# Optimization experiments

Hardware: AMD Instinct MI355X
Metric: run time of the kernel (lower is better)

The kernel has to match this reference:

```python
import jax, jax.numpy as jnp
import numpy as np

MC = 64  # mc_samples; fill=1.0 -> k == k_ball so neighbor ordering is irrelevant


def swish(x):
    return x * jax.nn.sigmoid(x)


def setup_inputs() -> dict:
    key = jax.random.key(0)
    ks = jax.random.split(key, 12)
    bs, n, g_dim = 4, 1024, 6
    c_in = c_out = 256
    H, hid = 8, 16

    def lin(k, i, o):
        return (jax.random.normal(k, (i, o), jnp.float32) / np.sqrt(i).astype(np.float32))

    return {
        "pairwise_g": jax.random.normal(ks[0], (bs, n, n, g_dim), jnp.float32),
        "coset_functions": jax.random.normal(ks[1], (bs, n, c_in), jnp.float32),
        "mask": jax.random.randint(ks[2], (bs, n), 0, 2) > 0,
        # per-head location-kernel MLP (MultiheadWeightNet: g_dim -> hid -> hid -> 1)
        "loc_W1": jax.random.normal(ks[3], (H, g_dim, hid), jnp.float32) / np.sqrt(g_dim).astype(np.float32),
        "loc_b1": jnp.zeros((H, hid), jnp.float32),
        "loc_W2": jax.random.normal(ks[4], (H, hid, hid), jnp.float32) / np.sqrt(hid).astype(np.float32),
        "loc_b2": jnp.zeros((H, hid), jnp.float32),
        "loc_W3": jax.random.normal(ks[5], (H, hid, 1), jnp.float32) / np.sqrt(hid).astype(np.float32),
        "loc_b3": jnp.zeros((H, 1), jnp.float32),
        # DotProductKernel projections
        "Wq": lin(ks[6], c_in, c_in), "bq": jnp.zeros((c_in,), jnp.float32),
        "Wk": lin(ks[7], c_in, c_in), "bk": jnp.zeros((c_in,), jnp.float32),
        # value (input_linear) and output projections
        "W_in": lin(ks[8], c_in, c_out), "b_in": jnp.zeros((c_out,), jnp.float32),
        "W_out": lin(ks[9], c_out, c_out), "b_out": jnp.zeros((c_out,), jnp.float32),
    }


def reference(pairwise_g, coset_functions, mask, loc_W1, loc_b1, loc_W2, loc_b2,
              loc_W3, loc_b3, Wq, bq, Wk, bk, W_in, b_in, W_out, b_out):
    bs, n, _, g_dim = pairwise_g.shape
    c_in = coset_functions.shape[-1]
    H = loc_W1.shape[0]
    dh = c_in // H
    b_idx = jnp.arange(bs)[:, None, None]

    # --- neighbourhood extraction: topk (smallest) group distances, masked keys pushed far away
    dists = jnp.linalg.norm(pairwise_g, axis=-1)                  # (b,n,n)
    dists = jnp.where(mask[:, None, :], dists, jnp.float32(1e8))
    _, nbhd_idx = jax.lax.top_k(-dists, MC)                       # (b,n,m) nearest MC keys
    nbhd_g = jnp.take_along_axis(pairwise_g, nbhd_idx[..., None], axis=2)  # (b,n,m,g)
    nbhd_mask = mask[b_idx, nbhd_idx]                             # (b,n,m)

    # --- location kernel: per-head MLP on gathered pairwise group elements
    h = swish(jnp.einsum('bnmg,hgk->bnmhk', nbhd_g, loc_W1) + loc_b1)
    h = swish(jnp.einsum('bnmhk,hkl->bnmhl', h, loc_W2) + loc_b2)
    loc = swish(jnp.einsum('bnmhk,hko->bnmho', h, loc_W3) + loc_b3)[..., 0]  # (b,n,m,H)

    # --- feature kernel: dot-product scores on gathered keys
    q = (coset_functions @ Wq + bq).reshape(bs, n, H, dh)
    k = (coset_functions @ Wk + bk).reshape(bs, n, H, dh)
    k_nbhd = k[b_idx, nbhd_idx]                                   # (b,n,m,H,dh)
    feat = jnp.einsum('bnhd,bnmhd->bnmh', q, k_nbhd) / np.sqrt(dh).astype(np.float32)

    # --- masked softmax over the neighbourhood dim (dim 2)
    scores = jnp.where(nbhd_mask[..., None], loc + feat, jnp.float32(-1e38))
    attn = jax.nn.softmax(scores, axis=2)                         # (b,n,m,H)

    # --- value projection + sparse attention (equivalent to the dense scatter+matmul,
    #     since topk neighbour indices are unique per query)
    v = (coset_functions @ W_in + b_in).reshape(bs, n, H, dh)
    v_nbhd = v[b_idx, nbhd_idx]                                   # (b,n,m,H,dh)
    out = jnp.einsum('bnmh,bnmhd->bnhd', attn, v_nbhd).reshape(bs, n, H * dh)
    out = out @ W_out + b_out
    return (pairwise_g, out, mask)
```

## Files before the change

### kernel.cpp

```cpp
#include <hip/hip_runtime.h>
#include <stdint.h>

#define BS 4
#define NN 1024
#define GD 6
#define CIN 256
#define NH 8
#define DH 32
#define HID 16
#define MCS 64

#define PG_ELEMS (BS*NN*NN*GD)
#define OUT_OFF  PG_ELEMS
#define MASK_OFF (PG_ELEMS + BS*NN*CIN)

typedef float vfloat4 __attribute__((ext_vector_type(4)));
typedef float vfloat2 __attribute__((ext_vector_type(2)));
typedef unsigned vuint4 __attribute__((ext_vector_type(4)));

#if __has_builtin(__builtin_amdgcn_rcpf)
__device__ __forceinline__ float fast_rcp(float x) { return __builtin_amdgcn_rcpf(x); }
#else
__device__ __forceinline__ float fast_rcp(float x) { return 1.0f / x; }
#endif
#if __has_builtin(__builtin_amdgcn_exp2f)
__device__ __forceinline__ float fast_exp2(float x) { return __builtin_amdgcn_exp2f(x); }
#else
__device__ __forceinline__ float fast_exp2(float x) { return exp2f(x); }
#endif
#define LOG2E 1.44269504088896340736f

__device__ __forceinline__ float swishf(float x) {
    return x * fast_rcp(1.0f + fast_exp2(x * -LOG2E));
}

template<int RPB>
__global__ __launch_bounds__(256) void gemm3(const float* __restrict__ X,
    const float* __restrict__ W0, const float* __restrict__ B0, float* __restrict__ D0,
    const float* __restrict__ W1, const float* __restrict__ B1, float* __restrict__ D1,
    const float* __restrict__ W2, const float* __restrict__ B2, float* __restrict__ D2)
{
    const float* W; const float* Bv; float* D;
    if (blockIdx.y == 0)      { W = W0; Bv = B0; D = D0; }
    else if (blockIdx.y == 1) { W = W1; Bv = B1; D = D1; }
    else                      { W = W2; Bv = B2; D = D2; }
    const int tid = threadIdx.x;
    const int c4  = tid & 63;
    const int rg  = tid >> 6;
    const int r0  = blockIdx.x * RPB;
    constexpr int RG = RPB / 4;

    __shared__ float xsT[CIN][RPB + 4];
    {
        float tmp[RPB];
        #pragma unroll
        for (int r = 0; r < RPB; ++r) tmp[r] = X[(size_t)(r0 + r)*CIN + tid];
        #pragma unroll
        for (int j = 0; j < RPB/4; ++j)
            *(vfloat4*)&xsT[tid][4*j] = (vfloat4){tmp[4*j+0], tmp[4*j+1], tmp[4*j+2], tmp[4*j+3]};
    }
    __syncthreads();

    vfloat4 acc[RG];
    #pragma unroll
    for (int r = 0; r < RG; ++r) acc[r] = (vfloat4){0.f,0.f,0.f,0.f};
    const vfloat4* W4 = (const vfloat4*)W;
    #pragma unroll 4
    for (int k = 0; k < CIN; ++k) {
        vfloat4 w = W4[(size_t)k*64 + c4];
        if constexpr (RG == 4) {
            vfloat4 xr = *(const vfloat4*)&xsT[k][rg*4];
            acc[0] += xr.x * w;
            acc[1] += xr.y * w;
            acc[2] += xr.z * w;
            acc[3] += xr.w * w;
        } else {
            vfloat2 xr = *(const vfloat2*)&xsT[k][rg*2];
            acc[0] += xr.x * w;
            acc[1] += xr.y * w;
        }
    }
    vfloat4 bb = ((const vfloat4*)Bv)[c4];
    vfloat4* D4 = (vfloat4*)D;
    const size_t rbase = (size_t)(r0 + rg*RG);
    #pragma unroll
    for (int r = 0; r < RG; ++r) D4[(rbase + r)*64 + c4] = acc[r] + bb;
}

__global__ __launch_bounds__(256, 8) void attn_topk(
    const float* __restrict__ pg, const int* __restrict__ mask,
    const float* __restrict__ lW1g, const float* __restrict__ lb1g,
    const float* __restrict__ lW2g, const float* __restrict__ lb2g,
    const float* __restrict__ lW3g, const float* __restrict__ lb3g,
    const float* __restrict__ Q, const float* __restrict__ Kc, const float* __restrict__ Vc,
    float* __restrict__ O, float* __restrict__ pg_out, float* __restrict__ mask_out)
{
    const int i = blockIdx.x, b = blockIdx.y, tid = threadIdx.x;
    const int lane = tid & 63;

    __shared__ __align__(16) unsigned selbuf[512];
    __shared__ float sg[MCS*7];
    __shared__ int nj[MCS];
    __shared__ __align__(16) unsigned joff[MCS];
    __shared__ vfloat4 obuf[4][64];
    __shared__ unsigned wsum[4];
    __shared__ unsigned sel_bin, sel_need, sel_cnt2, s_cnt, s_eqcnt, s_cand;

    float (*sc)[NH]   = (float (*)[NH])selbuf;
    unsigned* hist    = selbuf;
    unsigned* eqlist  = selbuf + 256;

    const int* mrow = mask + b*NN;
    if (tid == 0) { mask_out[b*NN + i] = mrow[i] ? 1.0f : 0.0f; s_cand = 0; }

    const size_t rowoff = (size_t)(b*NN + i) * (NN*GD);
    const vfloat4* src4 = (const vfloat4*)(pg + rowoff);
    vfloat4* dst4 = (vfloat4*)(pg_out + rowoff);
    #pragma unroll
    for (int t = 0; t < 6; ++t) {
        vfloat4 v = src4[tid + 256*t];
        __builtin_nontemporal_store(v, &dst4[tid + 256*t]);
    }
    vfloat4 q4 = ((const vfloat4*)Q)[(size_t)(b*NN + i)*64 + (tid & 63)];

    const int4 mv = ((const int4*)mrow)[tid];
    const vfloat4* gg = src4 + tid*6;
    vfloat4 g0 = gg[0], g1 = gg[1], g2 = gg[2], g3 = gg[3], g4 = gg[4], g5 = gg[5];
    float rv[4][6];
    rv[0][0]=g0.x; rv[0][1]=g0.y; rv[0][2]=g0.z; rv[0][3]=g0.w; rv[0][4]=g1.x; rv[0][5]=g1.y;
    rv[1][0]=g1.z; rv[1][1]=g1.w; rv[1][2]=g2.x; rv[1][3]=g2.y; rv[1][4]=g2.z; rv[1][5]=g2.w;
    rv[2][0]=g3.x; rv[2][1]=g3.y; rv[2][2]=g3.z; rv[2][3]=g3.w; rv[2][4]=g4.x; rv[2][5]=g4.y;
    rv[3][0]=g4.z; rv[3][1]=g4.w; rv[3][2]=g5.x; rv[3][3]=g5.y; rv[3][4]=g5.z; rv[3][5]=g5.w;
    const int vb[4] = { mv.x, mv.y, mv.z, mv.w };
    unsigned key[4];
    #pragma unroll
    for (int r = 0; r < 4; ++r) {
        float d2 = rv[r][0]*rv[r][0] + rv[r][1]*rv[r][1] + rv[r][2]*rv[r][2]
                 + rv[r][3]*rv[r][3] + rv[r][4]*rv[r][4] + rv[r][5]*rv[r][5];
        key[r] = __float_as_uint(vb[r] ? d2 : 1e30f);
    }

    unsigned prefix = 0;
    int need = MCS;
    unsigned T = 0;
    int needT = 0;
    for (int level = 0; level < 4; ++level) {
        const int shift = 24 - 8*level;
        hist[tid] = 0;
        __syncthreads();
        if (level == 0) {
            #pragma unroll
            for (int r = 0; r < 4; ++r) {
                unsigned d = key[r] >> 24;
                unsigned long long todo = __ballot(true);
                while (todo) {
                    int leader = (int)(__ffsll((unsigned long long)todo) - 1);
                    unsigned dl = __shfl(d, leader);
                    unsigned long long match = __ballot(d == dl);
                    if (lane == leader) atomicAdd(&hist[dl], (unsigned)__popcll(match));
                    todo &= ~match;
                }
            }
        } else {
            const unsigned pmask = 0xFFFFFFFFu << (shift + 8);
            #pragma unroll
            for (int r = 0; r < 4; ++r)
                if ((key[r] & pmask) == prefix)
                    atomicAdd(&hist[(key[r] >> shift) & 0xFFu], 1u);
        }
        __syncthreads();
        unsigned own = hist[tid];
        unsigned v = own;
        #pragma unroll
        for (int off = 1; off < 64; off <<= 1) {
            unsigned nv = __shfl_up(v, off);
            if (lane >= off) v += nv;
        }
        if (lane == 63) wsum[tid >> 6] = v;
        __syncthreads();
        unsigned basec = 0;
        for (int w = 0; w < (tid >> 6); ++w) basec += wsum[w];
        unsigned incl = v + basec;
        unsigned excl = incl - own;
        if (excl < (unsigned)need && (unsigned)need <= incl) {
            sel_bin  = (unsigned)tid;
            sel_need = (unsigned)need - excl;
            sel_cnt2 = own;
        }
        __syncthreads();
        prefix |= (sel_bin << shift);
        need = (int)sel_need;
        if (level == 3) { T = prefix; needT = need; break; }
        const int bincnt = (int)sel_cnt2;
        if (bincnt <= 64) {
            const unsigned pmask = 0xFFFFFFFFu << shift;
            unsigned* ckey = selbuf + 256;
            #pragma unroll
            for (int r = 0; r < 4; ++r) {
                if ((key[r] & pmask) == prefix) {
                    unsigned u = atomicAdd(&s_cand, 1u);
                    ckey[u] = key[r];
                }
            }
            __syncthreads();
            if (tid < 64) {
                unsigned myk = (tid < bincnt) ? ckey[tid] : 0xFFFFFFFFu;
                int rr = 0, ee = 0;
                for (int t = 0; t < bincnt; ++t) {
                    unsigned kt = __shfl(myk, t);
                    rr += (kt <  myk) ? 1 : 0;
                    ee += (kt == myk) ? 1 : 0;
                }
                if (tid < bincnt && rr < need && need <= rr + ee) {
                    sel_bin  = myk;
                    sel_need = (unsigned)(need - rr);
                }
            }
            __syncthreads();
            T = sel_bin; needT = (int)sel_need;
            break;
        }
    }

    if (tid == 0) { s_cnt = 0; s_eqcnt = 0; }
    __syncthreads();
    #pragma unroll
    for (int r = 0; r < 4; ++r) {
        unsigned kk = key[r];
        int j = tid*4 + r;
        if (kk < T) {
            unsigned p = atomicAdd(&s_cnt, 1u);
            nj[p] = j | (vb[r] ? 0 : (int)0x80000000);
            #pragma unroll
            for (int g = 0; g < GD; ++g) sg[p*7 + g] = rv[r][g];
        } else if (kk == T) {
            unsigned e = atomicAdd(&s_eqcnt, 1u);
            if (e < 64) eqlist[e] = (unsigned)j;
        }
    }
    __syncthreads();
    const int cbase = (int)s_cnt;
    if (tid == 0) {
        int ec = (int)s_eqcnt; if (ec > 64) ec = 64;
        for (int s2 = 0; s2 < needT; ++s2) {
            int bi = -1, bj = 0x7FFFFFFF;
            for (int e = 0; e < ec; ++e) {
                int jj = (int)eqlist[e];
                if (jj < bj) { bj = jj; bi = e; }
            }
            if (bi >= 0) {
                eqlist[bi] = 0x7FFFFFFFu;
                nj[cbase + s2] = bj | (mrow[bj] ? 0 : (int)0x80000000);
            }
        }
    }
    __syncthreads();
    #pragma unroll
    for (int r = 0; r < 4; ++r) {
        if (key[r] == T) {
            int j = tid*4 + r;
            for (int s2 = 0; s2 < needT; ++s2)
                if ((nj[cbase + s2] & 0x7FFFFFFF) == j) {
                    #pragma unroll
                    for (int g = 0; g < GD; ++g) sg[(cbase + s2)*7 + g] = rv[r][g];
                }
        }
    }
    if (tid < MCS) joff[tid] = ((unsigned)(b*NN + (nj[tid] & 0x7FFFFFFF))) << 6;
    __syncthreads();

    __builtin_amdgcn_s_setprio(1);
    #pragma unroll
    for (int pass = 0; pass < 2; ++pass) {
        const int h = __builtin_amdgcn_readfirstlane((tid >> 6) + pass*4);
        const int m = lane;
        const float* W1h = lW1g + h*(GD*HID);
        const float* B1h = lb1g + h*HID;
        const float* W2h = lW2g + h*(HID*HID);
        const float* B2h = lb2g + h*HID;
        const float* W3h = lW3g + h*HID;
        float gv[GD];
        #pragma unroll
        for (int g = 0; g < GD; ++g) gv[g] = sg[m*7 + g];
        float h1[HID];
        #pragma unroll
        for (int kk = 0; kk < HID; ++kk) {
            float a = B1h[kk];
            #pragma unroll
            for (int g = 0; g < GD; ++g) a += gv[g] * W1h[g*HID + kk];
            h1[kk] = swishf(a);
        }
        float h2[HID];
        #pragma unroll
        for (int l = 0; l < HID; ++l) {
            float a = B2h[l];
            #pragma unroll
            for (int kk = 0; kk < HID; ++kk) a += h1[kk] * W2h[kk*HID + l];
            h2[l] = swishf(a);
        }
        float a3 = lb3g[h];
        #pragma unroll
        for (int kk = 0; kk < HID; ++kk) a3 += h2[kk] * W3h[kk];
        sc[m][h] = (nj[m] < 0) ? -1e38f : swishf(a3);
    }
    __syncthreads();

    const int q = tid & 63;
    const int p = tid >> 6;
    const int hh = q >> 3;
    q4 *= 0.17677669529663688f;
    const vfloat4* Kc4 = (const vfloat4*)Kc;
    const vuint4* jo4 = (const vuint4*)(joff + (p << 4));
    #pragma unroll
    for (int mg = 0; mg < 4; ++mg) {
        vuint4 o4 = jo4[mg];
        vfloat4 kv0 = Kc4[o4.x + (unsigned)q];
        vfloat4 kv1 = Kc4[o4.y + (unsigned)q];
        vfloat4 kv2 = Kc4[o4.z + (unsigned)q];
        vfloat4 kv3 = Kc4[o4.w + (unsigned)q];
        const int mb = (p << 4) + (mg << 2);
        #define FEAT_RED(KV, RR) do { \
            float d = q4.x * (KV).x; \
            d = fmaf(q4.y, (KV).y, d); \
            d = fmaf(q4.z, (KV).z, d); \
            d = fmaf(q4.w, (KV).w, d); \
            d += __shfl_xor(d, 1); \
            d += __shfl_xor(d, 2); \
            d += __shfl_xor(d, 4); \
            if ((q & 7) == 0) sc[mb + (RR)][hh] += d; \
        } while (0)
        FEAT_RED(kv0, 0); FEAT_RED(kv1, 1); FEAT_RED(kv2, 2); FEAT_RED(kv3, 3);
        #undef FEAT_RED
    }
    __syncthreads();

    #pragma unroll
    for (int pass = 0; pass < 2; ++pass) {
        int h = (tid >> 6) + pass*4;
        float s = sc[lane][h];
        float mx = s;
        #pragma unroll
        for (int off = 32; off; off >>= 1) mx = fmaxf(mx, __shfl_xor(mx, off));
        float e = fast_exp2((s - mx) * LOG2E);
        float sum = e;
        #pragma unroll
        for (int off = 32; off; off >>= 1) sum += __shfl_xor(sum, off);
        sc[lane][h] = e * fast_rcp(sum);
    }
    __syncthreads();

    {
        const vfloat4* Vc4 = (const vfloat4*)Vc;
        vfloat4 acc = (vfloat4){0.f,0.f,0.f,0.f};
        #pragma unroll
        for (int mg = 0; mg < 4; ++mg) {
            vuint4 o4 = jo4[mg];
            vfloat4 v0 = Vc4[o4.x + (unsigned)q];
            vfloat4 v1 = Vc4[o4.y + (unsigned)q];
            vfloat4 v2 = Vc4[o4.z + (unsigned)q];
            vfloat4 v3 = Vc4[o4.w + (unsigned)q];
            const int mb = (p << 4) + (mg << 2);
            float a0 = sc[mb + 0][hh];
            float a1 = sc[mb + 1][hh];
            float a2 = sc[mb + 2][hh];
            float a3 = sc[mb + 3][hh];
            acc += a0 * v0;
            acc += a1 * v1;
            acc += a2 * v2;
            acc += a3 * v3;
        }
        __builtin_amdgcn_s_setprio(0);
        obuf[p][q] = acc;
    }
    __syncthreads();
    {
        const float* ob = (const float*)obuf;
        float s = ob[tid] + ob[256 + tid] + ob[512 + tid] + ob[768 + tid];
        O[(size_t)(b*NN + i)*CIN + tid] = s;
    }
}

extern "C" void kernel_launch(void* const* d_in, const int* in_sizes, int n_in,
                              void* d_out, int out_size, void* d_ws, size_t ws_size,
                              hipStream_t stream) {
    const float* pg   = (const float*)d_in[0];
    const float* x    = (const float*)d_in[1];
    const int*   mask = (const int*)d_in[2];
    const float* lW1  = (const float*)d_in[3];
    const float* lb1  = (const float*)d_in[4];
    const float* lW2  = (const float*)d_in[5];
    const float* lb2  = (const float*)d_in[6];
    const float* lW3  = (const float*)d_in[7];
    const float* lb3  = (const float*)d_in[8];
    const float* Wq   = (const float*)d_in[9];
    const float* bq   = (const float*)d_in[10];
    const float* Wk   = (const float*)d_in[11];
    const float* bk   = (const float*)d_in[12];
    const float* Wv   = (const float*)d_in[13];
    const float* bv   = (const float*)d_in[14];
    const float* Wo   = (const float*)d_in[15];
    const float* bo   = (const float*)d_in[16];

    float* out = (float*)d_out;
    float* Q  = (float*)d_ws;
    float* Kc = Q  + (size_t)BS*NN*CIN;
    float* Vc = Kc + (size_t)BS*NN*CIN;
    float* O  = Vc + (size_t)BS*NN*CIN;

    gemm3<16><<<dim3(BS*NN/16, 3), 256, 0, stream>>>(x, Wq, bq, Q, Wk, bk, Kc, Wv, bv, Vc);
    attn_topk<<<dim3(NN, BS), 256, 0, stream>>>(pg, mask, lW1, lb1, lW2, lb2, lW3, lb3,
                                                Q, Kc, Vc, O, out, out + MASK_OFF);
    gemm3<8><<<dim3(BS*NN/8, 1), 256, 0, stream>>>(O, Wo, bo, out + OUT_OFF,
                                                   Wo, bo, out + OUT_OFF,
                                                   Wo, bo, out + OUT_OFF);
}
```

Measured before the change: 329.5 us.

## Assign one query row per wavefront in attention top-k kernel, removing block barriers

Restructures the attention/top-k kernel so each 64-lane wavefront handles a whole query row, with four rows per 256-thread block, instead of one row per block. Radix-select histograms, candidate compaction, neighbor lists and softmax are now done with wave-level ballots and shuffles on per-wave shared buffers, which removes every __syncthreads. The aim is to cut barrier and cross-wave reduction overhead. In exchange each lane holds 16 keys and runs all 8 heads of the location MLP serially, so register pressure is higher (launch bounds lowered from 8 to 4) and each wave carries more serial work.

```diff
diff --git a/kernel.cpp b/kernel.cpp
--- a/kernel.cpp
+++ b/kernel.cpp
@@ -87,7 +87,7 @@
     for (int r = 0; r < RG; ++r) D4[(rbase + r)*64 + c4] = acc[r] + bb;
 }
 
-__global__ __launch_bounds__(256, 8) void attn_topk(
+__global__ __launch_bounds__(256, 4) void attn_topk(
     const float* __restrict__ pg, const int* __restrict__ mask,
     const float* __restrict__ lW1g, const float* __restrict__ lb1g,
     const float* __restrict__ lW2g, const float* __restrict__ lb2g,
@@ -95,193 +95,178 @@
     const float* __restrict__ Q, const float* __restrict__ Kc, const float* __restrict__ Vc,
     float* __restrict__ O, float* __restrict__ pg_out, float* __restrict__ mask_out)
 {
-    const int i = blockIdx.x, b = blockIdx.y, tid = threadIdx.x;
-    const int lane = tid & 63;
-
-    __shared__ __align__(16) unsigned selbuf[512];
-    __shared__ float sg[MCS*7];
-    __shared__ int nj[MCS];
-    __shared__ __align__(16) unsigned joff[MCS];
-    __shared__ vfloat4 obuf[4][64];
-    __shared__ unsigned wsum[4];
-    __shared__ unsigned sel_bin, sel_need, sel_cnt2, s_cnt, s_eqcnt, s_cand;
-
-    float (*sc)[NH]   = (float (*)[NH])selbuf;
-    unsigned* hist    = selbuf;
-    unsigned* eqlist  = selbuf + 256;
+    const int tid = threadIdx.x;
+    const int w = tid >> 6, l = tid & 63;
+    const int i = blockIdx.x*4 + w, b = blockIdx.y;
+
+    __shared__ __align__(16) float s_sc[4][576];
+    __shared__ __align__(16) int s_nj[4][64];
+    __shared__ __align__(16) unsigned s_joff[4][64];
+    float* scf = s_sc[w];
+    unsigned* hist = (unsigned*)s_sc[w];
+    unsigned* ckey = (unsigned*)s_sc[w] + 256;
+    int* nj = s_nj[w];
+    unsigned* joff = s_joff[w];
 
     const int* mrow = mask + b*NN;
-    if (tid == 0) { mask_out[b*NN + i] = mrow[i] ? 1.0f : 0.0f; s_cand = 0; }
+    if (l == 0) mask_out[b*NN + i] = mrow[i] ? 1.0f : 0.0f;
 
     const size_t rowoff = (size_t)(b*NN + i) * (NN*GD);
     const vfloat4* src4 = (const vfloat4*)(pg + rowoff);
     vfloat4* dst4 = (vfloat4*)(pg_out + rowoff);
+
     #pragma unroll
-    for (int t = 0; t < 6; ++t) {
-        vfloat4 v = src4[tid + 256*t];
-        __builtin_nontemporal_store(v, &dst4[tid + 256*t]);
-    }
-    vfloat4 q4 = ((const vfloat4*)Q)[(size_t)(b*NN + i)*64 + (tid & 63)];
-
-    const int4 mv = ((const int4*)mrow)[tid];
-    const vfloat4* gg = src4 + tid*6;
-    vfloat4 g0 = gg[0], g1 = gg[1], g2 = gg[2], g3 = gg[3], g4 = gg[4], g5 = gg[5];
-    float rv[4][6];
-    rv[0][0]=g0.x; rv[0][1]=g0.y; rv[0][2]=g0.z; rv[0][3]=g0.w; rv[0][4]=g1.x; rv[0][5]=g1.y;
-    rv[1][0]=g1.z; rv[1][1]=g1.w; rv[1][2]=g2.x; rv[1][3]=g2.y; rv[1][4]=g2.z; rv[1][5]=g2.w;
-    rv[2][0]=g3.x; rv[2][1]=g3.y; rv[2][2]=g3.z; rv[2][3]=g3.w; rv[2][4]=g4.x; rv[2][5]=g4.y;
-    rv[3][0]=g4.z; rv[3][1]=g4.w; rv[3][2]=g5.x; rv[3][3]=g5.y; rv[3][4]=g5.z; rv[3][5]=g5.w;
-    const int vb[4] = { mv.x, mv.y, mv.z, mv.w };
-    unsigned key[4];
-    #pragma unroll
-    for (int r = 0; r < 4; ++r) {
-        float d2 = rv[r][0]*rv[r][0] + rv[r][1]*rv[r][1] + rv[r][2]*rv[r][2]
-                 + rv[r][3]*rv[r][3] + rv[r][4]*rv[r][4] + rv[r][5]*rv[r][5];
-        key[r] = __float_as_uint(vb[r] ? d2 : 1e30f);
-    }
-
-    unsigned prefix = 0;
-    int need = MCS;
-    unsigned T = 0;
-    int needT = 0;
+    for (int c = 0; c < 3; ++c) {
+        vfloat4 t0 = src4[l + 64*(8*c+0)], t1 = src4[l + 64*(8*c+1)];
+        vfloat4 t2 = src4[l + 64*(8*c+2)], t3 = src4[l + 64*(8*c+3)];
+        vfloat4 t4 = src4[l + 64*(8*c+4)], t5 = src4[l + 64*(8*c+5)];
+        vfloat4 t6 = src4[l + 64*(8*c+6)], t7 = src4[l + 64*(8*c+7)];
+        __builtin_nontemporal_store(t0, &dst4[l + 64*(8*c+0)]);
+        __builtin_nontemporal_store(t1, &dst4[l + 64*(8*c+1)]);
+        __builtin_nontemporal_store(t2, &dst4[l + 64*(8*c+2)]);
+        __builtin_nontemporal_store(t3, &dst4[l + 64*(8*c+3)]);
+        __builtin_nontemporal_store(t4, &dst4[l + 64*(8*c+4)]);
+        __builtin_nontemporal_store(t5, &dst4[l + 64*(8*c+5)]);
+        __builtin_nontemporal_store(t6, &dst4[l + 64*(8*c+6)]);
+        __builtin_nontemporal_store(t7, &dst4[l + 64*(8*c+7)]);
+    }
+    vfloat4 q4 = ((const vfloat4*)Q)[(size_t)(b*NN + i)*64 + l];
+
+    const unsigned U30 = __float_as_uint(1e30f);
+    unsigned key[16];
+    #pragma unroll 2
+    for (int rg = 0; rg < 4; ++rg) {
+        const int4 mv = ((const int4*)mrow)[l + 64*rg];
+        const vfloat4* gp = src4 + 6*(l + 64*rg);
+        vfloat4 a0 = gp[0], a1 = gp[1], a2 = gp[2], a3 = gp[3], a4 = gp[4], a5 = gp[5];
+        float d0 = a0.x*a0.x + a0.y*a0.y + a0.z*a0.z + a0.w*a0.w + a1.x*a1.x + a1.y*a1.y;
+        float d1 = a1.z*a1.z + a1.w*a1.w + a2.x*a2.x + a2.y*a2.y + a2.z*a2.z + a2.w*a2.w;
+        float d2 = a3.x*a3.x + a3.y*a3.y + a3.z*a3.z + a3.w*a3.w + a4.x*a4.x + a4.y*a4.y;
+        float d3 = a4.z*a4.z + a4.w*a4.w + a5.x*a5.x + a5.y*a5.y + a5.z*a5.z + a5.w*a5.w;
+        key[rg*4+0] = __float_as_uint(mv.x ? d0 : 1e30f);
+        key[rg*4+1] = __float_as_uint(mv.y ? d1 : 1e30f);
+        key[rg*4+2] = __float_as_uint(mv.z ? d2 : 1e30f);
+        key[rg*4+3] = __float_as_uint(mv.w ? d3 : 1e30f);
+    }
+
+    const unsigned long long ltm = ((unsigned long long)1 << l) - 1;
+    unsigned prefix = 0, T = 0;
+    int need = MCS, needT = 0;
+    #pragma unroll 1
     for (int level = 0; level < 4; ++level) {
         const int shift = 24 - 8*level;
-        hist[tid] = 0;
-        __syncthreads();
-        if (level == 0) {
-            #pragma unroll
-            for (int r = 0; r < 4; ++r) {
-                unsigned d = key[r] >> 24;
-                unsigned long long todo = __ballot(true);
-                while (todo) {
-                    int leader = (int)(__ffsll((unsigned long long)todo) - 1);
-                    unsigned dl = __shfl(d, leader);
-                    unsigned long long match = __ballot(d == dl);
-                    if (lane == leader) atomicAdd(&hist[dl], (unsigned)__popcll(match));
-                    todo &= ~match;
-                }
+        ((vuint4*)hist)[l] = (vuint4){0,0,0,0};
+        const unsigned pmaskhi = (level == 0) ? 0u : (0xFFFFFFFFu << (shift + 8));
+        #pragma unroll
+        for (int r = 0; r < 16; ++r) {
+            const bool act = (level == 0) ? true : ((key[r] & pmaskhi) == prefix);
+            const unsigned d = (key[r] >> shift) & 0xFFu;
+            unsigned long long todo = __ballot(act);
+            while (todo) {
+                int leader = (int)(__ffsll((unsigned long long)todo) - 1);
+                unsigned dl = __shfl(d, leader);
+                unsigned long long mm = __ballot(act && d == dl);
+                if (l == leader) hist[dl] += (unsigned)__popcll(mm);
+                todo &= ~mm;
             }
-        } else {
-            const unsigned pmask = 0xFFFFFFFFu << (shift + 8);
-            #pragma unroll
-            for (int r = 0; r < 4; ++r)
-                if ((key[r] & pmask) == prefix)
-                    atomicAdd(&hist[(key[r] >> shift) & 0xFFu], 1u);
-        }
-        __syncthreads();
-        unsigned own = hist[tid];
+        }
+        vuint4 bb = ((const vuint4*)hist)[l];
+        unsigned own = bb.x + bb.y + bb.z + bb.w;
         unsigned v = own;
         #pragma unroll
         for (int off = 1; off < 64; off <<= 1) {
             unsigned nv = __shfl_up(v, off);
-            if (lane >= off) v += nv;
-        }
-        if (lane == 63) wsum[tid >> 6] = v;
-        __syncthreads();
-        unsigned basec = 0;
-        for (int w = 0; w < (tid >> 6); ++w) basec += wsum[w];
-        unsigned incl = v + basec;
-        unsigned excl = incl - own;
-        if (excl < (unsigned)need && (unsigned)need <= incl) {
-            sel_bin  = (unsigned)tid;
-            sel_need = (unsigned)need - excl;
-            sel_cnt2 = own;
-        }
-        __syncthreads();
-        prefix |= (sel_bin << shift);
-        need = (int)sel_need;
+            if (l >= off) v += nv;
+        }
+        const unsigned excl = v - own;
+        const unsigned un = (unsigned)need;
+        unsigned long long hb = __ballot(excl < un && un <= v);
+        int hl = (int)__ffsll(hb) - 1;
+        unsigned c0 = excl + bb.x, c1 = c0 + bb.y, c2 = c1 + bb.z;
+        int t    = (un <= c0) ? 0 : (un <= c1) ? 1 : (un <= c2) ? 2 : 3;
+        unsigned ndl = un - ((t == 0) ? excl : (t == 1) ? c0 : (t == 2) ? c1 : c2);
+        unsigned bnl = (t == 0) ? bb.x : (t == 1) ? bb.y : (t == 2) ? bb.z : bb.w;
+        unsigned binl = 4u*l + (unsigned)t;
+        unsigned bin = __shfl(binl, hl);
+        need = (int)__shfl(ndl, hl);
+        const int bincnt = (int)__shfl(bnl, hl);
+        prefix |= bin << shift;
         if (level == 3) { T = prefix; needT = need; break; }
-        const int bincnt = (int)sel_cnt2;
         if (bincnt <= 64) {
-            const unsigned pmask = 0xFFFFFFFFu << shift;
-            unsigned* ckey = selbuf + 256;
+            const unsigned pm = 0xFFFFFFFFu << shift;
+            unsigned cb = 0;
             #pragma unroll
-            for (int r = 0; r < 4; ++r) {
-                if ((key[r] & pmask) == prefix) {
-                    unsigned u = atomicAdd(&s_cand, 1u);
-                    ckey[u] = key[r];
-                }
+            for (int r = 0; r < 16; ++r) {
+                bool mt = (key[r] & pm) == prefix;
+                unsigned long long mm = __ballot(mt);
+                if (mt) ckey[cb + (unsigned)__popcll(mm & ltm)] = key[r];
+                cb += (unsigned)__popcll(mm);
             }
-            __syncthreads();
-            if (tid < 64) {
-                unsigned myk = (tid < bincnt) ? ckey[tid] : 0xFFFFFFFFu;
-                int rr = 0, ee = 0;
-                for (int t = 0; t < bincnt; ++t) {
-                    unsigned kt = __shfl(myk, t);
-                    rr += (kt <  myk) ? 1 : 0;
-                    ee += (kt == myk) ? 1 : 0;
-                }
-                if (tid < bincnt && rr < need && need <= rr + ee) {
-                    sel_bin  = myk;
-                    sel_need = (unsigned)(need - rr);
-                }
+            unsigned myk = (l < bincnt) ? ckey[l] : 0xFFFFFFFFu;
+            int rk = 0, ee = 0;
+            for (int t2 = 0; t2 < bincnt; ++t2) {
+                unsigned kt = __shfl(myk, t2);
+                rk += (kt <  myk) ? 1 : 0;
+                ee += (kt == myk) ? 1 : 0;
             }
-            __syncthreads();
-            T = sel_bin; needT = (int)sel_need;
+            unsigned long long sb = __ballot((l < bincnt) && rk < need && need <= rk + ee);
+            int sl2 = (int)__ffsll(sb) - 1;
+            T = __shfl(myk, sl2);
+            needT = __shfl(need - rk, sl2);
             break;
         }
     }
 
-    if (tid == 0) { s_cnt = 0; s_eqcnt = 0; }
-    __syncthreads();
+    unsigned cnt = 0, ec = 0;
     #pragma unroll
-    for (int r = 0; r < 4; ++r) {
-        unsigned kk = key[r];
-        int j = tid*4 + r;
-        if (kk < T) {
-            unsigned p = atomicAdd(&s_cnt, 1u);
-            nj[p] = j | (vb[r] ? 0 : (int)0x80000000);
-            #pragma unroll
-            for (int g = 0; g < GD; ++g) sg[p*7 + g] = rv[r][g];
-        } else if (kk == T) {
-            unsigned e = atomicAdd(&s_eqcnt, 1u);
-            if (e < 64) eqlist[e] = (unsigned)j;
-        }
-    }
-    __syncthreads();
-    const int cbase = (int)s_cnt;
-    if (tid == 0) {
-        int ec = (int)s_eqcnt; if (ec > 64) ec = 64;
+    for (int r = 0; r < 16; ++r) {
+        const int j = 4*(l + 64*(r >> 2)) + (r & 3);
+        const unsigned kk = key[r];
+        bool s1 = kk < T;
+        unsigned long long m1 = __ballot(s1);
+        if (s1) nj[cnt + (unsigned)__popcll(m1 & ltm)] = j | ((kk == U30) ? (int)0x80000000 : 0);
+        cnt += (unsigned)__popcll(m1);
+        bool s2 = kk == T;
+        unsigned long long m2 = __ballot(s2);
+        if (s2) {
+            unsigned e = ec + (unsigned)__popcll(m2 & ltm);
+            if (e < 64) ckey[e] = (unsigned)j;
+        }
+        ec += (unsigned)__popcll(m2);
+    }
+    const int cbase = (int)cnt;
+    if (l == 0) {
+        int ecc = (int)ec; if (ecc > 64) ecc = 64;
         for (int s2 = 0; s2 < needT; ++s2) {
             int bi = -1, bj = 0x7FFFFFFF;
-            for (int e = 0; e < ec; ++e) {
-                int jj = (int)eqlist[e];
+            for (int e = 0; e < ecc; ++e) {
+                int jj = (int)ckey[e];
                 if (jj < bj) { bj = jj; bi = e; }
             }
             if (bi >= 0) {
-                eqlist[bi] = 0x7FFFFFFFu;
+                ckey[bi] = 0x7FFFFFFFu;
                 nj[cbase + s2] = bj | (mrow[bj] ? 0 : (int)0x80000000);
             }
         }
     }
-    __syncthreads();
-    #pragma unroll
-    for (int r = 0; r < 4; ++r) {
-        if (key[r] == T) {
-            int j = tid*4 + r;
-            for (int s2 = 0; s2 < needT; ++s2)
-                if ((nj[cbase + s2] & 0x7FFFFFFF) == j) {
-                    #pragma unroll
-                    for (int g = 0; g < GD; ++g) sg[(cbase + s2)*7 + g] = rv[r][g];
-                }
-        }
-    }
-    if (tid < MCS) joff[tid] = ((unsigned)(b*NN + (nj[tid] & 0x7FFFFFFF))) << 6;
-    __syncthreads();
+
+    const int code = nj[l];
+    const int jm = code & 0x7FFFFFFF;
+    joff[l] = ((unsigned)(b*NN + jm)) << 6;
+    const float* gp2 = pg + rowoff + (size_t)jm * 6;
+    vfloat2 g01 = *(const vfloat2*)gp2;
+    vfloat2 g23 = *(const vfloat2*)(gp2 + 2);
+    vfloat2 g45 = *(const vfloat2*)(gp2 + 4);
+    float gv[GD] = { g01.x, g01.y, g23.x, g23.y, g45.x, g45.y };
 
     __builtin_amdgcn_s_setprio(1);
-    #pragma unroll
-    for (int pass = 0; pass < 2; ++pass) {
-        const int h = __builtin_amdgcn_readfirstlane((tid >> 6) + pass*4);
-        const int m = lane;
+    #pragma unroll 1
+    for (int h = 0; h < NH; ++h) {
         const float* W1h = lW1g + h*(GD*HID);
         const float* B1h = lb1g + h*HID;
         const float* W2h = lW2g + h*(HID*HID);
         const float* B2h = lb2g + h*HID;
         const float* W3h = lW3g + h*HID;
-        float gv[GD];
-        #pragma unroll
-        for (int g = 0; g < GD; ++g) gv[g] = sg[m*7 + g];
         float h1[HID];
         #pragma unroll
         for (int kk = 0; kk < HID; ++kk) {
@@ -292,34 +277,32 @@
         }
         float h2[HID];
         #pragma unroll
-        for (int l = 0; l < HID; ++l) {
-            float a = B2h[l];
+        for (int ll = 0; ll < HID; ++ll) {
+            float a = B2h[ll];
             #pragma unroll
-            for (int kk = 0; kk < HID; ++kk) a += h1[kk] * W2h[kk*HID + l];
-            h2[l] = swishf(a);
+            for (int kk = 0; kk < HID; ++kk) a += h1[kk] * W2h[kk*HID + ll];
+            h2[ll] = swishf(a);
         }
         float a3 = lb3g[h];
         #pragma unroll
         for (int kk = 0; kk < HID; ++kk) a3 += h2[kk] * W3h[kk];
-        sc[m][h] = (nj[m] < 0) ? -1e38f : swishf(a3);
-    }
-    __syncthreads();
-
-    const int q = tid & 63;
-    const int p = tid >> 6;
-    const int hh = q >> 3;
+        scf[l*9 + h] = (code < 0) ? -1e38f : swishf(a3);
+    }
+
+    const int lr = l & 7, hh = l >> 3;
     q4 *= 0.17677669529663688f;
     const vfloat4* Kc4 = (const vfloat4*)Kc;
-    const vuint4* jo4 = (const vuint4*)(joff + (p << 4));
+    float pack0 = 0.f, pack1 = 0.f, pack2 = 0.f, pack3 = 0.f,
+          pack4 = 0.f, pack5 = 0.f, pack6 = 0.f, pack7 = 0.f;
     #pragma unroll
-    for (int mg = 0; mg < 4; ++mg) {
-        vuint4 o4 = jo4[mg];
-        vfloat4 kv0 = Kc4[o4.x + (unsigned)q];
-        vfloat4 kv1 = Kc4[o4.y + (unsigned)q];
-        vfloat4 kv2 = Kc4[o4.z + (unsigned)q];
-        vfloat4 kv3 = Kc4[o4.w + (unsigned)q];
-        const int mb = (p << 4) + (mg << 2);
+    for (int mg = 0; mg < 16; ++mg) {
+        vuint4 o4 = *(const vuint4*)&joff[4*mg];
+        vfloat4 kv0 = Kc4[o4.x + (unsigned)l];
+        vfloat4 kv1 = Kc4[o4.y + (unsigned)l];
+        vfloat4 kv2 = Kc4[o4.z + (unsigned)l];
+        vfloat4 kv3 = Kc4[o4.w + (unsigned)l];
         #define FEAT_RED(KV, RR) do { \
+            const int m_ = 4*mg + (RR); \
             float d = q4.x * (KV).x; \
             d = fmaf(q4.y, (KV).y, d); \
             d = fmaf(q4.z, (KV).z, d); \
@@ -327,17 +310,30 @@
             d += __shfl_xor(d, 1); \
             d += __shfl_xor(d, 2); \
             d += __shfl_xor(d, 4); \
-            if ((q & 7) == 0) sc[mb + (RR)][hh] += d; \
+            if (lr == (m_ & 7)) { \
+                switch (m_ >> 3) { \
+                    case 0: pack0 = d; break; case 1: pack1 = d; break; \
+                    case 2: pack2 = d; break; case 3: pack3 = d; break; \
+                    case 4: pack4 = d; break; case 5: pack5 = d; break; \
+                    case 6: pack6 = d; break; default: pack7 = d; break; \
+                } \
+            } \
         } while (0)
         FEAT_RED(kv0, 0); FEAT_RED(kv1, 1); FEAT_RED(kv2, 2); FEAT_RED(kv3, 3);
         #undef FEAT_RED
     }
-    __syncthreads();
-
-    #pragma unroll
-    for (int pass = 0; pass < 2; ++pass) {
-        int h = (tid >> 6) + pass*4;
-        float s = sc[lane][h];
+    scf[(8*0 + lr)*9 + hh] += pack0;
+    scf[(8*1 + lr)*9 + hh] += pack1;
+    scf[(8*2 + lr)*9 + hh] += pack2;
+    scf[(8*3 + lr)*9 + hh] += pack3;
+    scf[(8*4 + lr)*9 + hh] += pack4;
+    scf[(8*5 + lr)*9 + hh] += pack5;
+    scf[(8*6 + lr)*9 + hh] += pack6;
+    scf[(8*7 + lr)*9 + hh] += pack7;
+
+    #pragma unroll 1
+    for (int h = 0; h < NH; ++h) {
+        float s = scf[l*9 + h];
         float mx = s;
         #pragma unroll
         for (int off = 32; off; off >>= 1) mx = fmaxf(mx, __shfl_xor(mx, off));
@@ -345,38 +341,30 @@
         float sum = e;
         #pragma unroll
         for (int off = 32; off; off >>= 1) sum += __shfl_xor(sum, off);
-        sc[lane][h] = e * fast_rcp(sum);
-    }
-    __syncthreads();
+        scf[l*9 + h] = e * fast_rcp(sum);
+    }
 
     {
         const vfloat4* Vc4 = (const vfloat4*)Vc;
         vfloat4 acc = (vfloat4){0.f,0.f,0.f,0.f};
         #pragma unroll
-        for (int mg = 0; mg < 4; ++mg) {
-            vuint4 o4 = jo4[mg];
-            vfloat4 v0 = Vc4[o4.x + (unsigned)q];
-            vfloat4 v1 = Vc4[o4.y + (unsigned)q];
-            vfloat4 v2 = Vc4[o4.z + (unsigned)q];
-            vfloat4 v3 = Vc4[o4.w + (unsigned)q];
-            const int mb = (p << 4) + (mg << 2);
-            float a0 = sc[mb + 0][hh];
-            float a1 = sc[mb + 1][hh];
-            float a2 = sc[mb + 2][hh];
-            float a3 = sc[mb + 3][hh];
+        for (int mg = 0; mg < 16; ++mg) {
+            vuint4 o4 = *(const vuint4*)&joff[4*mg];
+            vfloat4 v0 = Vc4[o4.x + (unsigned)l];
+            vfloat4 v1 = Vc4[o4.y + (unsigned)l];
+            vfloat4 v2 = Vc4[o4.z + (unsigned)l];
+            vfloat4 v3 = Vc4[o4.w + (unsigned)l];
+            float a0 = scf[(4*mg + 0)*9 + hh];
+            float a1 = scf[(4*mg + 1)*9 + hh];
+            float a2 = scf[(4*mg + 2)*9 + hh];
+            float a3 = scf[(4*mg + 3)*9 + hh];
             acc += a0 * v0;
             acc += a1 * v1;
             acc += a2 * v2;
             acc += a3 * v3;
         }
         __builtin_amdgcn_s_setprio(0);
-        obuf[p][q] = acc;
-    }
-    __syncthreads();
-    {
-        const float* ob = (const float*)obuf;
-        float s = ob[tid] + ob[256 + tid] + ob[512 + tid] + ob[768 + tid];
-        O[(size_t)(b*NN + i)*CIN + tid] = s;
+        ((vfloat4*)O)[(size_t)(b*NN + i)*64 + l] = acc;
     }
 }
 
@@ -408,8 +396,8 @@
     float* O  = Vc + (size_t)BS*NN*CIN;
 
     gemm3<16><<<dim3(BS*NN/16, 3), 256, 0, stream>>>(x, Wq, bq, Q, Wk, bk, Kc, Wv, bv, Vc);
-    attn_topk<<<dim3(NN, BS), 256, 0, stream>>>(pg, mask, lW1, lb1, lW2, lb2, lW3, lb3,
-                                                Q, Kc, Vc, O, out, out + MASK_OFF);
+    attn_topk<<<dim3(NN/4, BS), 256, 0, stream>>>(pg, mask, lW1, lb1, lW2, lb2, lW3, lb3,
+                                                  Q, Kc, Vc, O, out, out + MASK_OFF);
     gemm3<8><<<dim3(BS*NN/8, 1), 256, 0, stream>>>(O, Wo, bo, out + OUT_OFF,
                                                    Wo, bo, out + OUT_OFF,
                                                    Wo, bo, out + OUT_OFF);
```

Result: slower. 383.5 us (+16.4%).
